# Kernel tuning notes

Measured on AMD Instinct MI355X. Metric: run time of the kernel, lower is better.

Reference implementation:

```python
import jax, jax.numpy as jnp
import numpy as np

B, LQ, LK, D = 16, 2048, 2048, 256
NEG = -1e10


def setup_inputs() -> dict:
    key = jax.random.key(0)
    k1, k2, k3, k4, k5 = jax.random.split(key, 5)
    scale = 1.0 / np.sqrt(D)
    return {
        "x": jax.random.normal(k1, (B, LQ, D), dtype=jnp.float32),
        "y": jax.random.normal(k2, (B, LK, D), dtype=jnp.float32),
        "mask": jnp.zeros((B, LK), dtype=bool),  # True = padded key position
        "Wq": jax.random.normal(k3, (D, D), dtype=jnp.float32) * scale,
        "Wk": jax.random.normal(k4, (D, D), dtype=jnp.float32) * scale,
        "Wv": jax.random.normal(k5, (D, D), dtype=jnp.float32) * scale,
    }


def reference(x, y, mask, Wq, Wk, Wv):
    # nn.Linear: out = in @ W.T (no bias)
    q = jnp.einsum('bqd,ed->bqe', x, Wq)   # [B, LQ, D]
    k = jnp.einsum('bkd,ed->bke', y, Wk)   # [B, LK, D]
    v = jnp.einsum('bkd,ed->bke', y, Wv)   # [B, LK, D]
    # cdist (p=2) via GEMM expansion: ||q||^2 + ||k||^2 - 2 q.k
    qn = jnp.sum(q * q, axis=-1)                              # [B, LQ]
    kn = jnp.sum(k * k, axis=-1)                              # [B, LK]
    d2 = qn[:, :, None] + kn[:, None, :] - 2.0 * jnp.einsum('bqd,bkd->bqk', q, k)
    dist = jnp.sqrt(jnp.maximum(d2, 0.0))                     # [B, LQ, LK]
    scores = jnp.exp(-dist)
    # masked_fill: where original mask is True, set pre-softmax score to -1e10
    scores = jnp.where(mask[:, None, :], NEG, scores)
    attn = jax.nn.softmax(scores, axis=-1)                    # [B, LQ, LK]
    att_out = jnp.einsum('bqk,bkd->bqd', attn, v)             # [B, LQ, D]
    return (att_out, attn)
```

## Files before the change

kernel.cpp:

```cpp
#include <hip/hip_runtime.h>
#include <stdint.h>

#define B_   16
#define L_   2048
#define D_   256
#define NROW (B_*L_)

#define EPAD 40
#define TPAD 66

typedef __attribute__((ext_vector_type(8))) short s8v;
typedef __attribute__((ext_vector_type(4))) float f4v;

__device__ __forceinline__ unsigned short f2b(float f) {
    unsigned u = __builtin_bit_cast(unsigned, f);
    return (unsigned short)((u + 0x7fffu + ((u >> 16) & 1u)) >> 16);
}

__device__ __forceinline__ void gl16(const void* g, void* l) {
    __builtin_amdgcn_global_load_lds(
        (const __attribute__((address_space(1))) unsigned int*)g,
        (__attribute__((address_space(3))) unsigned int*)l, 16, 0, 0);
}

__global__ __launch_bounds__(256) void qkv_kernel(
    const float* __restrict__ x, const float* __restrict__ y,
    const float* __restrict__ Wq, const float* __restrict__ Wk, const float* __restrict__ Wv,
    unsigned short* __restrict__ Qb, unsigned short* __restrict__ Kb,
    unsigned short* __restrict__ Vt,
    float* __restrict__ qn, float* __restrict__ kn)
{
    __shared__ unsigned short Xs[64*256];
    __shared__ unsigned short Ws[64*256];
    __shared__ unsigned short Ts[64*TPAD];

    const int t    = threadIdx.x;
    const int r0   = blockIdx.x * 64;
    const int type = blockIdx.y;

    const float* X = type ? y : x;

    #pragma unroll
    for (int p = 0; p < 16; ++p) {
        int idx  = p*256 + t;
        int row  = idx >> 6;
        int half = idx & 1;
        int blk  = (idx & 63) >> 1;
        int c4   = blk*8 + half*4;
        float4 vx = *(const float4*)(X + (size_t)(r0+row)*D_ + c4);
        uint2 px;
        px.x = (unsigned)f2b(vx.x) | ((unsigned)f2b(vx.y) << 16);
        px.y = (unsigned)f2b(vx.z) | ((unsigned)f2b(vx.w) << 16);
        *(uint2*)(Xs + row*256 + (blk ^ (row & 15))*8 + half*4) = px;
    }

    const int w = t >> 6, lane = t & 63, q16 = lane & 15, quad = lane >> 4;
    const int m0 = w * 16;

    float p4[4] = {0.f, 0.f, 0.f, 0.f};
    const f4v z4 = {0.f, 0.f, 0.f, 0.f};

    for (int ct = 0; ct < 4; ++ct) {
        const int e0 = ct * 64;

        __syncthreads();
        {
            const float* W = type ? Wk : Wq;
            #pragma unroll
            for (int p = 0; p < 16; ++p) {
                int idx  = p*256 + t;
                int row  = idx >> 6;
                int half = idx & 1;
                int blk  = (idx & 63) >> 1;
                int c4   = blk*8 + half*4;
                float4 vw = *(const float4*)(W + (size_t)(e0+row)*D_ + c4);
                uint2 pw;
                pw.x = (unsigned)f2b(vw.x) | ((unsigned)f2b(vw.y) << 16);
                pw.y = (unsigned)f2b(vw.z) | ((unsigned)f2b(vw.w) << 16);
                *(uint2*)(Ws + row*256 + (blk ^ (row & 15))*8 + half*4) = pw;
            }
        }
        __syncthreads();

        f4v acc[4];
        #pragma unroll
        for (int n = 0; n < 4; ++n) acc[n] = z4;
        #pragma unroll
        for (int c = 0; c < 8; ++c) {
            s8v a = *(const s8v*)(Xs + (m0 + q16)*256 + (((c*4+quad) ^ q16)*8));
            #pragma unroll
            for (int n = 0; n < 4; ++n) {
                s8v bb = *(const s8v*)(Ws + (n*16 + q16)*256 + (((c*4+quad) ^ q16)*8));
                acc[n] = __builtin_amdgcn_mfma_f32_16x16x32_bf16(a, bb, acc[n], 0, 0, 0);
            }
        }
        {
            unsigned short* Out = type ? Kb : Qb;
            #pragma unroll
            for (int n = 0; n < 4; ++n)
                #pragma unroll
                for (int r = 0; r < 4; ++r) {
                    float v = acc[n][r];
                    p4[r] += v * v;
                    Out[(size_t)(r0 + m0 + quad*4 + r)*D_ + e0 + n*16 + q16] = f2b(v);
                }
        }

        if (type) {
            __syncthreads();
            #pragma unroll
            for (int p = 0; p < 16; ++p) {
                int idx  = p*256 + t;
                int row  = idx >> 6;
                int half = idx & 1;
                int blk  = (idx & 63) >> 1;
                int c4   = blk*8 + half*4;
                float4 vw = *(const float4*)(Wv + (size_t)(e0+row)*D_ + c4);
                uint2 pw;
                pw.x = (unsigned)f2b(vw.x) | ((unsigned)f2b(vw.y) << 16);
                pw.y = (unsigned)f2b(vw.z) | ((unsigned)f2b(vw.w) << 16);
                *(uint2*)(Ws + row*256 + (blk ^ (row & 15))*8 + half*4) = pw;
            }
            __syncthreads();

            f4v vacc[4];
            #pragma unroll
            for (int n = 0; n < 4; ++n) vacc[n] = z4;
            #pragma unroll
            for (int c = 0; c < 8; ++c) {
                s8v a = *(const s8v*)(Xs + (m0 + q16)*256 + (((c*4+quad) ^ q16)*8));
                #pragma unroll
                for (int n = 0; n < 4; ++n) {
                    s8v bb = *(const s8v*)(Ws + (n*16 + q16)*256 + (((c*4+quad) ^ q16)*8));
                    vacc[n] = __builtin_amdgcn_mfma_f32_16x16x32_bf16(a, bb, vacc[n], 0, 0, 0);
                }
            }
            #pragma unroll
            for (int n = 0; n < 4; ++n)
                #pragma unroll
                for (int r = 0; r < 4; ++r)
                    Ts[(m0 + quad*4 + r)*TPAD + n*16 + q16] = f2b(vacc[n][r]);
            __syncthreads();
            int j    = t >> 2;
            int kseg = t & 3;
            unsigned pk[8];
            #pragma unroll
            for (int i = 0; i < 8; ++i) {
                unsigned lo = Ts[(kseg*16 + 2*i    )*TPAD + j];
                unsigned hi = Ts[(kseg*16 + 2*i + 1)*TPAD + j];
                pk[i] = lo | (hi << 16);
            }
            int bb_ = r0 >> 11;
            int k0g = r0 & (L_ - 1);
            unsigned short* dst = Vt + (size_t)(bb_*D_ + e0 + j)*L_ + k0g + kseg*16;
            *(uint4*)dst       = make_uint4(pk[0], pk[1], pk[2], pk[3]);
            *((uint4*)dst + 1) = make_uint4(pk[4], pk[5], pk[6], pk[7]);
        }
    }

    {
        float* norm = type ? kn : qn;
        #pragma unroll
        for (int r = 0; r < 4; ++r) {
            float v = p4[r];
            v += __shfl_xor(v, 1, 16);
            v += __shfl_xor(v, 2, 16);
            v += __shfl_xor(v, 4, 16);
            v += __shfl_xor(v, 8, 16);
            if (q16 == 0) norm[r0 + m0 + quad*4 + r] = v;
        }
    }
}

__device__ __forceinline__ void stage_K(const unsigned short* Kb, unsigned short* ks,
                                        int bk, int k0, int w, int lane) {
    #pragma unroll
    for (int p = 0; p < 4; ++p) {
        int slot = p*256 + w*64 + lane;
        int row  = slot >> 5;
        int blk  = slot & 31;
        gl16(Kb + (size_t)(bk + k0 + row)*D_ + ((blk ^ (row & 15))*8),
             ks + (size_t)(p*256 + w*64)*8);
    }
}
__device__ __forceinline__ void stage_V(const unsigned short* Vt, unsigned short* vs,
                                        int bD, int k0, int w, int lane) {
    #pragma unroll
    for (int p = 0; p < 4; ++p) {
        int slot = p*256 + w*64 + lane;
        int d    = slot >> 2;
        int blk  = slot & 3;
        gl16(Vt + (size_t)(bD + d)*L_ + k0 + ((blk ^ ((d >> 1) & 3))*8),
             vs + (size_t)(p*256 + w*64)*8);
    }
}

__global__ __launch_bounds__(256) void attnpv_kernel(
    const unsigned short* __restrict__ Qb, const unsigned short* __restrict__ Kb,
    const unsigned short* __restrict__ Vt,
    const float* __restrict__ qn, const float* __restrict__ kn,
    const unsigned char* __restrict__ mask,
    unsigned short* __restrict__ Eb,
    float* __restrict__ rowsum, float* __restrict__ att_out)
{
    __shared__ unsigned short Ks[2][32*256];
    __shared__ unsigned short Vs[2][256*32];
    __shared__ unsigned short Es[4][16*EPAD];

    const int t  = threadIdx.x;
    const int q0 = blockIdx.x * 64;
    const int b  = blockIdx.y;
    const int bk = b * L_;
    const int bD = b * D_;
    const int w = t >> 6, lane = t & 63, q16 = lane & 15, quad = lane >> 4;

    const int qrow = bk + q0 + w*16;
    s8v qa[8];
    float qnr[4];
    #pragma unroll
    for (int c = 0; c < 8; ++c)
        qa[c] = *(const s8v*)(Qb + (size_t)(qrow + q16)*D_ + c*32 + quad*8);
    #pragma unroll
    for (int r = 0; r < 4; ++r)
        qnr[r] = qn[qrow + quad*4 + r];

    unsigned short* ebase = Eb + (size_t)(qrow + (lane >> 2))*L_ + (lane & 3)*8;
    const unsigned short* esrc = &Es[w][(lane >> 2)*EPAD + (lane & 3)*8];

    float rs[4] = {0.f, 0.f, 0.f, 0.f};
    const f4v z4 = {0.f, 0.f, 0.f, 0.f};
    f4v O[16];
    #pragma unroll
    for (int n = 0; n < 16; ++n) O[n] = z4;

    stage_K(Kb, Ks[0], bk, 0, w, lane);
    stage_V(Vt, Vs[0], bD, 0, w, lane);
    for (int kt = 0; kt < 64; ++kt) {
        const int k0 = kt * 32;
        const int cur = kt & 1;
        __syncthreads();
        if (kt < 63) {
            stage_K(Kb, Ks[cur ^ 1], bk, k0 + 32, w, lane);
            stage_V(Vt, Vs[cur ^ 1], bD, k0 + 32, w, lane);
        }

        float kcv[2]; int mkv[2];
        #pragma unroll
        for (int n = 0; n < 2; ++n) {
            kcv[n] = kn[bk + k0 + n*16 + q16];
            mkv[n] = mask[bk + k0 + n*16 + q16];
        }

        #pragma unroll
        for (int n = 0; n < 2; ++n) {
            f4v s = {0.f, 0.f, 0.f, 0.f};
            #pragma unroll
            for (int c = 0; c < 8; ++c) {
                s8v bb = *(const s8v*)(Ks[cur] + (n*16 + q16)*256 + (((c*4+quad) ^ q16)*8));
                s = __builtin_amdgcn_mfma_f32_16x16x32_bf16(qa[c], bb, s, 0, 0, 0);
            }
            #pragma unroll
            for (int r = 0; r < 4; ++r) {
                float d2 = qnr[r] + kcv[n] - 2.0f * s[r];
                float dist = sqrtf(fmaxf(d2, 0.f));
                float E = mkv[n] ? 0.f : __expf(__expf(-dist));
                rs[r] += E;
                Es[w][(quad*4 + r)*EPAD + n*16 + q16] = f2b(E);
            }
        }
        s8v af = *(const s8v*)(&Es[w][q16*EPAD + quad*8]);
        #pragma unroll
        for (int n = 0; n < 16; ++n) {
            s8v vb = *(const s8v*)(Vs[cur] + (n*16 + q16)*32 +
                                   ((quad ^ ((q16 >> 1) & 3))*8));
            O[n] = __builtin_amdgcn_mfma_f32_16x16x32_bf16(af, vb, O[n], 0, 0, 0);
        }
        *(s8v*)(ebase + k0) = *(const s8v*)esrc;
    }

    float inv[4];
    #pragma unroll
    for (int r = 0; r < 4; ++r) {
        float v = rs[r];
        v += __shfl_xor(v, 1, 16);
        v += __shfl_xor(v, 2, 16);
        v += __shfl_xor(v, 4, 16);
        v += __shfl_xor(v, 8, 16);
        if (q16 == 0) rowsum[qrow + quad*4 + r] = v;
        inv[r] = 1.0f / v;
    }

    #pragma unroll
    for (int n = 0; n < 16; ++n)
        #pragma unroll
        for (int r = 0; r < 4; ++r)
            att_out[(size_t)(qrow + quad*4 + r)*D_ + n*16 + q16] = O[n][r] * inv[r];
}

__global__ __launch_bounds__(256) void norm_kernel(
    const unsigned short* __restrict__ Eb,
    const float* __restrict__ rowsum,
    float* __restrict__ attn_out)
{
    const int row = blockIdx.x;
    const int t   = threadIdx.x;
    const float inv = 1.0f / rowsum[row];
    const size_t base = (size_t)row * L_ + t*8;

    s8v e = *(const s8v*)(Eb + base);
    float4 o0, o1;
    o0.x = __builtin_bit_cast(float, ((unsigned)(unsigned short)e[0]) << 16) * inv;
    o0.y = __builtin_bit_cast(float, ((unsigned)(unsigned short)e[1]) << 16) * inv;
    o0.z = __builtin_bit_cast(float, ((unsigned)(unsigned short)e[2]) << 16) * inv;
    o0.w = __builtin_bit_cast(float, ((unsigned)(unsigned short)e[3]) << 16) * inv;
    o1.x = __builtin_bit_cast(float, ((unsigned)(unsigned short)e[4]) << 16) * inv;
    o1.y = __builtin_bit_cast(float, ((unsigned)(unsigned short)e[5]) << 16) * inv;
    o1.z = __builtin_bit_cast(float, ((unsigned)(unsigned short)e[6]) << 16) * inv;
    o1.w = __builtin_bit_cast(float, ((unsigned)(unsigned short)e[7]) << 16) * inv;
    *(float4*)(attn_out + base)     = o0;
    *(float4*)(attn_out + base + 4) = o1;
}

extern "C" void kernel_launch(void* const* d_in, const int* in_sizes, int n_in,
                              void* d_out, int out_size, void* d_ws, size_t ws_size,
                              hipStream_t stream) {
    (void)in_sizes; (void)n_in; (void)out_size; (void)ws_size;
    const float* x  = (const float*)d_in[0];
    const float* y  = (const float*)d_in[1];
    const unsigned char* mask = (const unsigned char*)d_in[2];
    const float* Wq = (const float*)d_in[3];
    const float* Wk = (const float*)d_in[4];
    const float* Wv = (const float*)d_in[5];

    char* ws = (char*)d_ws;
    unsigned short* Qb = (unsigned short*)ws;
    unsigned short* Kb = Qb + (size_t)NROW * D_;
    unsigned short* Vt = Kb + (size_t)NROW * D_;
    float* qn     = (float*)(ws + 3 * (size_t)NROW * D_ * 2);
    float* kn     = qn + NROW;
    float* rowsum = kn + NROW;
    unsigned short* Eb = (unsigned short*)(rowsum + NROW);

    float* att_out = (float*)d_out;
    float* attn    = att_out + (size_t)NROW * D_;

    qkv_kernel<<<dim3(512, 2), 256, 0, stream>>>(x, y, Wq, Wk, Wv,
                                                 Qb, Kb, Vt, qn, kn);
    attnpv_kernel<<<dim3(32, 16), 256, 0, stream>>>(Qb, Kb, Vt, qn, kn, mask,
                                                    Eb, rowsum, att_out);
    norm_kernel<<<dim3(NROW), 256, 0, stream>>>(Eb, rowsum, attn);
}
```

Measured before the change: 592.1 us.

## Fuse attention normalization into attn kernel, remap blocks, add hardware bf16 packing

Drops the separate norm kernel. Each attention block now re-reads its own bf16 exp rows from the workspace after the main loop and writes the normalized fp32 attention matrix with nontemporal stores. It also remaps block indices to interleave batches, raises wave priority around the MFMA loops, and replaces software bf16 rounding in the projection kernel with the v_cvt_pk_bf16_f32 instruction. The intent is to remove a launch and the rowsum round trip, and to lower conversion ALU cost. The cost is that the large attention write now sits in the tail of a 512-block kernel and may serialize with compute.

```diff
diff --git a/kernel.cpp b/kernel.cpp
--- a/kernel.cpp
+++ b/kernel.cpp
@@ -11,10 +11,17 @@
 
 typedef __attribute__((ext_vector_type(8))) short s8v;
 typedef __attribute__((ext_vector_type(4))) float f4v;
+typedef __attribute__((ext_vector_type(4))) float f4n;
 
 __device__ __forceinline__ unsigned short f2b(float f) {
     unsigned u = __builtin_bit_cast(unsigned, f);
     return (unsigned short)((u + 0x7fffu + ((u >> 16) & 1u)) >> 16);
+}
+
+__device__ __forceinline__ unsigned cvtpk(float a, float b) {
+    unsigned r;
+    asm("v_cvt_pk_bf16_f32 %0, %1, %2" : "=v"(r) : "v"(a), "v"(b));
+    return r;
 }
 
 __device__ __forceinline__ void gl16(const void* g, void* l) {
@@ -49,8 +56,8 @@
         int c4   = blk*8 + half*4;
         float4 vx = *(const float4*)(X + (size_t)(r0+row)*D_ + c4);
         uint2 px;
-        px.x = (unsigned)f2b(vx.x) | ((unsigned)f2b(vx.y) << 16);
-        px.y = (unsigned)f2b(vx.z) | ((unsigned)f2b(vx.w) << 16);
+        px.x = cvtpk(vx.x, vx.y);
+        px.y = cvtpk(vx.z, vx.w);
         *(uint2*)(Xs + row*256 + (blk ^ (row & 15))*8 + half*4) = px;
     }
 
@@ -75,8 +82,8 @@
                 int c4   = blk*8 + half*4;
                 float4 vw = *(const float4*)(W + (size_t)(e0+row)*D_ + c4);
                 uint2 pw;
-                pw.x = (unsigned)f2b(vw.x) | ((unsigned)f2b(vw.y) << 16);
-                pw.y = (unsigned)f2b(vw.z) | ((unsigned)f2b(vw.w) << 16);
+                pw.x = cvtpk(vw.x, vw.y);
+                pw.y = cvtpk(vw.z, vw.w);
                 *(uint2*)(Ws + row*256 + (blk ^ (row & 15))*8 + half*4) = pw;
             }
         }
@@ -117,8 +124,8 @@
                 int c4   = blk*8 + half*4;
                 float4 vw = *(const float4*)(Wv + (size_t)(e0+row)*D_ + c4);
                 uint2 pw;
-                pw.x = (unsigned)f2b(vw.x) | ((unsigned)f2b(vw.y) << 16);
-                pw.y = (unsigned)f2b(vw.z) | ((unsigned)f2b(vw.w) << 16);
+                pw.x = cvtpk(vw.x, vw.y);
+                pw.y = cvtpk(vw.z, vw.w);
                 *(uint2*)(Ws + row*256 + (blk ^ (row & 15))*8 + half*4) = pw;
             }
             __syncthreads();
@@ -201,15 +208,17 @@
     const float* __restrict__ qn, const float* __restrict__ kn,
     const unsigned char* __restrict__ mask,
     unsigned short* __restrict__ Eb,
-    float* __restrict__ rowsum, float* __restrict__ att_out)
+    float* __restrict__ att_out, float* __restrict__ attn)
 {
     __shared__ unsigned short Ks[2][32*256];
     __shared__ unsigned short Vs[2][256*32];
     __shared__ unsigned short Es[4][16*EPAD];
+    __shared__ float invsh[4][16];
 
     const int t  = threadIdx.x;
-    const int q0 = blockIdx.x * 64;
-    const int b  = blockIdx.y;
+    const int s  = blockIdx.y * 32 + blockIdx.x;
+    const int b  = ((s & 7) << 1) | (s >> 8);
+    const int q0 = ((s >> 3) & 31) * 64;
     const int bk = b * L_;
     const int bD = b * D_;
     const int w = t >> 6, lane = t & 63, q16 = lane & 15, quad = lane >> 4;
@@ -253,15 +262,17 @@
 
         #pragma unroll
         for (int n = 0; n < 2; ++n) {
-            f4v s = {0.f, 0.f, 0.f, 0.f};
+            f4v s4 = {0.f, 0.f, 0.f, 0.f};
+            __builtin_amdgcn_s_setprio(1);
             #pragma unroll
             for (int c = 0; c < 8; ++c) {
                 s8v bb = *(const s8v*)(Ks[cur] + (n*16 + q16)*256 + (((c*4+quad) ^ q16)*8));
-                s = __builtin_amdgcn_mfma_f32_16x16x32_bf16(qa[c], bb, s, 0, 0, 0);
-            }
+                s4 = __builtin_amdgcn_mfma_f32_16x16x32_bf16(qa[c], bb, s4, 0, 0, 0);
+            }
+            __builtin_amdgcn_s_setprio(0);
             #pragma unroll
             for (int r = 0; r < 4; ++r) {
-                float d2 = qnr[r] + kcv[n] - 2.0f * s[r];
+                float d2 = qnr[r] + kcv[n] - 2.0f * s4[r];
                 float dist = sqrtf(fmaxf(d2, 0.f));
                 float E = mkv[n] ? 0.f : __expf(__expf(-dist));
                 rs[r] += E;
@@ -269,16 +280,18 @@
             }
         }
         s8v af = *(const s8v*)(&Es[w][q16*EPAD + quad*8]);
+        __builtin_amdgcn_s_setprio(1);
         #pragma unroll
         for (int n = 0; n < 16; ++n) {
             s8v vb = *(const s8v*)(Vs[cur] + (n*16 + q16)*32 +
                                    ((quad ^ ((q16 >> 1) & 3))*8));
             O[n] = __builtin_amdgcn_mfma_f32_16x16x32_bf16(af, vb, O[n], 0, 0, 0);
         }
+        __builtin_amdgcn_s_setprio(0);
         *(s8v*)(ebase + k0) = *(const s8v*)esrc;
     }
 
-    float inv[4];
+    float inv4[4];
     #pragma unroll
     for (int r = 0; r < 4; ++r) {
         float v = rs[r];
@@ -286,39 +299,41 @@
         v += __shfl_xor(v, 2, 16);
         v += __shfl_xor(v, 4, 16);
         v += __shfl_xor(v, 8, 16);
-        if (q16 == 0) rowsum[qrow + quad*4 + r] = v;
-        inv[r] = 1.0f / v;
+        inv4[r] = 1.0f / v;
+        if (q16 == 0) invsh[w][quad*4 + r] = inv4[r];
     }
 
     #pragma unroll
     for (int n = 0; n < 16; ++n)
         #pragma unroll
         for (int r = 0; r < 4; ++r)
-            att_out[(size_t)(qrow + quad*4 + r)*D_ + n*16 + q16] = O[n][r] * inv[r];
-}
-
-__global__ __launch_bounds__(256) void norm_kernel(
-    const unsigned short* __restrict__ Eb,
-    const float* __restrict__ rowsum,
-    float* __restrict__ attn_out)
-{
-    const int row = blockIdx.x;
-    const int t   = threadIdx.x;
-    const float inv = 1.0f / rowsum[row];
-    const size_t base = (size_t)row * L_ + t*8;
-
-    s8v e = *(const s8v*)(Eb + base);
-    float4 o0, o1;
-    o0.x = __builtin_bit_cast(float, ((unsigned)(unsigned short)e[0]) << 16) * inv;
-    o0.y = __builtin_bit_cast(float, ((unsigned)(unsigned short)e[1]) << 16) * inv;
-    o0.z = __builtin_bit_cast(float, ((unsigned)(unsigned short)e[2]) << 16) * inv;
-    o0.w = __builtin_bit_cast(float, ((unsigned)(unsigned short)e[3]) << 16) * inv;
-    o1.x = __builtin_bit_cast(float, ((unsigned)(unsigned short)e[4]) << 16) * inv;
-    o1.y = __builtin_bit_cast(float, ((unsigned)(unsigned short)e[5]) << 16) * inv;
-    o1.z = __builtin_bit_cast(float, ((unsigned)(unsigned short)e[6]) << 16) * inv;
-    o1.w = __builtin_bit_cast(float, ((unsigned)(unsigned short)e[7]) << 16) * inv;
-    *(float4*)(attn_out + base)     = o0;
-    *(float4*)(attn_out + base + 4) = o1;
+            __builtin_nontemporal_store(O[n][r] * inv4[r],
+                att_out + (size_t)(qrow + quad*4 + r)*D_ + n*16 + q16);
+
+    __syncthreads();
+
+    {
+        const int rloc = lane >> 2, cseg = lane & 3;
+        const float invr = invsh[w][rloc];
+        const unsigned short* erow = Eb + (size_t)(qrow + rloc)*L_;
+        float* arow = attn + (size_t)(qrow + rloc)*L_;
+        #pragma unroll 4
+        for (int it = 0; it < 64; ++it) {
+            const int c0 = it*32 + cseg*8;
+            s8v e = *(const s8v*)(erow + c0);
+            f4n o0, o1;
+            o0.x = __builtin_bit_cast(float, ((unsigned)(unsigned short)e[0]) << 16) * invr;
+            o0.y = __builtin_bit_cast(float, ((unsigned)(unsigned short)e[1]) << 16) * invr;
+            o0.z = __builtin_bit_cast(float, ((unsigned)(unsigned short)e[2]) << 16) * invr;
+            o0.w = __builtin_bit_cast(float, ((unsigned)(unsigned short)e[3]) << 16) * invr;
+            o1.x = __builtin_bit_cast(float, ((unsigned)(unsigned short)e[4]) << 16) * invr;
+            o1.y = __builtin_bit_cast(float, ((unsigned)(unsigned short)e[5]) << 16) * invr;
+            o1.z = __builtin_bit_cast(float, ((unsigned)(unsigned short)e[6]) << 16) * invr;
+            o1.w = __builtin_bit_cast(float, ((unsigned)(unsigned short)e[7]) << 16) * invr;
+            __builtin_nontemporal_store(o0, (f4n*)(arow + c0));
+            __builtin_nontemporal_store(o1, (f4n*)(arow + c0 + 4));
+        }
+    }
 }
 
 extern "C" void kernel_launch(void* const* d_in, const int* in_sizes, int n_in,
@@ -338,8 +353,7 @@
     unsigned short* Vt = Kb + (size_t)NROW * D_;
     float* qn     = (float*)(ws + 3 * (size_t)NROW * D_ * 2);
     float* kn     = qn + NROW;
-    float* rowsum = kn + NROW;
-    unsigned short* Eb = (unsigned short*)(rowsum + NROW);
+    unsigned short* Eb = (unsigned short*)(kn + NROW);
 
     float* att_out = (float*)d_out;
     float* attn    = att_out + (size_t)NROW * D_;
@@ -347,6 +361,5 @@
     qkv_kernel<<<dim3(512, 2), 256, 0, stream>>>(x, y, Wq, Wk, Wv,
                                                  Qb, Kb, Vt, qn, kn);
     attnpv_kernel<<<dim3(32, 16), 256, 0, stream>>>(Qb, Kb, Vt, qn, kn, mask,
-                                                    Eb, rowsum, att_out);
-    norm_kernel<<<dim3(NROW), 256, 0, stream>>>(Eb, rowsum, attn);
-}
+                                                    Eb, att_out, attn);
+}
```

After: 605.6 us. +2.3%, slower.

## Triple-buffer attention tiles with 512-thread blocks, LDS kn/mask, and nontemporal stores

Applied to the files above, without the earlier changes.

Several changes land together. The attention kernel grows to 512 threads covering 128 query rows and moves to a three-stage K/V LDS pipeline with explicit vmcnt waits and barriers. Key norms and mask go into shared memory, block indices are remapped to interleave batches, and MFMA sections get raised priority with s_setprio. Separately, bf16 conversion switches to the packed v_cvt_pk_bf16_f32 instruction, and the output stores become nontemporal. The extra LDS and the hand-written waitcnt logic may reduce occupancy or risk ordering bugs.

```diff
diff --git a/kernel.cpp b/kernel.cpp
--- a/kernel.cpp
+++ b/kernel.cpp
@@ -11,10 +11,17 @@
 
 typedef __attribute__((ext_vector_type(8))) short s8v;
 typedef __attribute__((ext_vector_type(4))) float f4v;
+typedef __attribute__((ext_vector_type(4))) float f4n;
 
 __device__ __forceinline__ unsigned short f2b(float f) {
     unsigned u = __builtin_bit_cast(unsigned, f);
     return (unsigned short)((u + 0x7fffu + ((u >> 16) & 1u)) >> 16);
+}
+
+__device__ __forceinline__ unsigned cvtpk(float a, float b) {
+    unsigned r;
+    asm("v_cvt_pk_bf16_f32 %0, %1, %2" : "=v"(r) : "v"(a), "v"(b));
+    return r;
 }
 
 __device__ __forceinline__ void gl16(const void* g, void* l) {
@@ -49,8 +56,8 @@
         int c4   = blk*8 + half*4;
         float4 vx = *(const float4*)(X + (size_t)(r0+row)*D_ + c4);
         uint2 px;
-        px.x = (unsigned)f2b(vx.x) | ((unsigned)f2b(vx.y) << 16);
-        px.y = (unsigned)f2b(vx.z) | ((unsigned)f2b(vx.w) << 16);
+        px.x = cvtpk(vx.x, vx.y);
+        px.y = cvtpk(vx.z, vx.w);
         *(uint2*)(Xs + row*256 + (blk ^ (row & 15))*8 + half*4) = px;
     }
 
@@ -75,8 +82,8 @@
                 int c4   = blk*8 + half*4;
                 float4 vw = *(const float4*)(W + (size_t)(e0+row)*D_ + c4);
                 uint2 pw;
-                pw.x = (unsigned)f2b(vw.x) | ((unsigned)f2b(vw.y) << 16);
-                pw.y = (unsigned)f2b(vw.z) | ((unsigned)f2b(vw.w) << 16);
+                pw.x = cvtpk(vw.x, vw.y);
+                pw.y = cvtpk(vw.z, vw.w);
                 *(uint2*)(Ws + row*256 + (blk ^ (row & 15))*8 + half*4) = pw;
             }
         }
@@ -117,8 +124,8 @@
                 int c4   = blk*8 + half*4;
                 float4 vw = *(const float4*)(Wv + (size_t)(e0+row)*D_ + c4);
                 uint2 pw;
-                pw.x = (unsigned)f2b(vw.x) | ((unsigned)f2b(vw.y) << 16);
-                pw.y = (unsigned)f2b(vw.z) | ((unsigned)f2b(vw.w) << 16);
+                pw.x = cvtpk(vw.x, vw.y);
+                pw.y = cvtpk(vw.z, vw.w);
                 *(uint2*)(Ws + row*256 + (blk ^ (row & 15))*8 + half*4) = pw;
             }
             __syncthreads();
@@ -175,27 +182,27 @@
 __device__ __forceinline__ void stage_K(const unsigned short* Kb, unsigned short* ks,
                                         int bk, int k0, int w, int lane) {
     #pragma unroll
-    for (int p = 0; p < 4; ++p) {
-        int slot = p*256 + w*64 + lane;
+    for (int p = 0; p < 2; ++p) {
+        int slot = p*512 + w*64 + lane;
         int row  = slot >> 5;
         int blk  = slot & 31;
         gl16(Kb + (size_t)(bk + k0 + row)*D_ + ((blk ^ (row & 15))*8),
-             ks + (size_t)(p*256 + w*64)*8);
+             ks + (size_t)(p*512 + w*64)*8);
     }
 }
 __device__ __forceinline__ void stage_V(const unsigned short* Vt, unsigned short* vs,
                                         int bD, int k0, int w, int lane) {
     #pragma unroll
-    for (int p = 0; p < 4; ++p) {
-        int slot = p*256 + w*64 + lane;
+    for (int p = 0; p < 2; ++p) {
+        int slot = p*512 + w*64 + lane;
         int d    = slot >> 2;
         int blk  = slot & 3;
         gl16(Vt + (size_t)(bD + d)*L_ + k0 + ((blk ^ ((d >> 1) & 3))*8),
-             vs + (size_t)(p*256 + w*64)*8);
-    }
-}
-
-__global__ __launch_bounds__(256) void attnpv_kernel(
+             vs + (size_t)(p*512 + w*64)*8);
+    }
+}
+
+__global__ __launch_bounds__(512) void attnpv_kernel(
     const unsigned short* __restrict__ Qb, const unsigned short* __restrict__ Kb,
     const unsigned short* __restrict__ Vt,
     const float* __restrict__ qn, const float* __restrict__ kn,
@@ -203,18 +210,24 @@
     unsigned short* __restrict__ Eb,
     float* __restrict__ rowsum, float* __restrict__ att_out)
 {
-    __shared__ unsigned short Ks[2][32*256];
-    __shared__ unsigned short Vs[2][256*32];
-    __shared__ unsigned short Es[4][16*EPAD];
+    __shared__ unsigned short Ks[3][32*256];
+    __shared__ unsigned short Vs[3][256*32];
+    __shared__ unsigned short Es[8][16*EPAD];
+    __shared__ float         knS[L_];
+    __shared__ unsigned char mkS[L_];
 
     const int t  = threadIdx.x;
-    const int q0 = blockIdx.x * 64;
-    const int b  = blockIdx.y;
+    const int s  = blockIdx.y * 16 + blockIdx.x;
+    const int b  = ((s & 7) << 1) | (s >> 7);
+    const int q0 = ((s >> 3) & 15) * 128;
     const int bk = b * L_;
     const int bD = b * D_;
     const int w = t >> 6, lane = t & 63, q16 = lane & 15, quad = lane >> 4;
-
     const int qrow = bk + q0 + w*16;
+
+    *(float4*)&knS[t*4] = *(const float4*)&kn[bk + t*4];
+    ((unsigned*)mkS)[t] = ((const unsigned*)(mask + bk))[t];
+
     s8v qa[8];
     float qnr[4];
     #pragma unroll
@@ -233,35 +246,27 @@
     #pragma unroll
     for (int n = 0; n < 16; ++n) O[n] = z4;
 
-    stage_K(Kb, Ks[0], bk, 0, w, lane);
-    stage_V(Vt, Vs[0], bD, 0, w, lane);
-    for (int kt = 0; kt < 64; ++kt) {
+    auto do_tile = [&](int kt, int cur) {
         const int k0 = kt * 32;
-        const int cur = kt & 1;
-        __syncthreads();
-        if (kt < 63) {
-            stage_K(Kb, Ks[cur ^ 1], bk, k0 + 32, w, lane);
-            stage_V(Vt, Vs[cur ^ 1], bD, k0 + 32, w, lane);
-        }
-
         float kcv[2]; int mkv[2];
         #pragma unroll
         for (int n = 0; n < 2; ++n) {
-            kcv[n] = kn[bk + k0 + n*16 + q16];
-            mkv[n] = mask[bk + k0 + n*16 + q16];
-        }
-
+            kcv[n] = knS[k0 + n*16 + q16];
+            mkv[n] = mkS[k0 + n*16 + q16];
+        }
         #pragma unroll
         for (int n = 0; n < 2; ++n) {
-            f4v s = {0.f, 0.f, 0.f, 0.f};
+            f4v s4 = z4;
+            __builtin_amdgcn_s_setprio(1);
             #pragma unroll
             for (int c = 0; c < 8; ++c) {
                 s8v bb = *(const s8v*)(Ks[cur] + (n*16 + q16)*256 + (((c*4+quad) ^ q16)*8));
-                s = __builtin_amdgcn_mfma_f32_16x16x32_bf16(qa[c], bb, s, 0, 0, 0);
-            }
+                s4 = __builtin_amdgcn_mfma_f32_16x16x32_bf16(qa[c], bb, s4, 0, 0, 0);
+            }
+            __builtin_amdgcn_s_setprio(0);
             #pragma unroll
             for (int r = 0; r < 4; ++r) {
-                float d2 = qnr[r] + kcv[n] - 2.0f * s[r];
+                float d2 = fmaf(-2.0f, s4[r], qnr[r] + kcv[n]);
                 float dist = sqrtf(fmaxf(d2, 0.f));
                 float E = mkv[n] ? 0.f : __expf(__expf(-dist));
                 rs[r] += E;
@@ -269,16 +274,41 @@
             }
         }
         s8v af = *(const s8v*)(&Es[w][q16*EPAD + quad*8]);
+        __builtin_amdgcn_s_setprio(1);
         #pragma unroll
         for (int n = 0; n < 16; ++n) {
             s8v vb = *(const s8v*)(Vs[cur] + (n*16 + q16)*32 +
                                    ((quad ^ ((q16 >> 1) & 3))*8));
             O[n] = __builtin_amdgcn_mfma_f32_16x16x32_bf16(af, vb, O[n], 0, 0, 0);
         }
+        __builtin_amdgcn_s_setprio(0);
         *(s8v*)(ebase + k0) = *(const s8v*)esrc;
-    }
-
-    float inv[4];
+    };
+
+    stage_K(Kb, Ks[0], bk, 0,  w, lane);  stage_V(Vt, Vs[0], bD, 0,  w, lane);
+    stage_K(Kb, Ks[1], bk, 32, w, lane);  stage_V(Vt, Vs[1], bD, 32, w, lane);
+
+    asm volatile("s_waitcnt vmcnt(4) lgkmcnt(0)\n\ts_barrier" ::: "memory");
+    do_tile(0, 0);
+    asm volatile("s_barrier" ::: "memory");
+    stage_K(Kb, Ks[2], bk, 64, w, lane);  stage_V(Vt, Vs[2], bD, 64, w, lane);
+
+    int cur = 1;
+    for (int kt = 1; kt <= 62; ++kt) {
+        asm volatile("s_waitcnt vmcnt(5)\n\ts_barrier" ::: "memory");
+        do_tile(kt, cur);
+        asm volatile("s_barrier" ::: "memory");
+        if (kt <= 61) {
+            int nb = cur - 1; if (nb < 0) nb = 2;
+            stage_K(Kb, Ks[nb], bk, (kt+2)*32, w, lane);
+            stage_V(Vt, Vs[nb], bD, (kt+2)*32, w, lane);
+        }
+        cur = (cur == 2) ? 0 : cur + 1;
+    }
+    asm volatile("s_waitcnt vmcnt(1)\n\ts_barrier" ::: "memory");
+    do_tile(63, 0);
+
+    float inv4[4];
     #pragma unroll
     for (int r = 0; r < 4; ++r) {
         float v = rs[r];
@@ -286,15 +316,15 @@
         v += __shfl_xor(v, 2, 16);
         v += __shfl_xor(v, 4, 16);
         v += __shfl_xor(v, 8, 16);
+        inv4[r] = 1.0f / v;
         if (q16 == 0) rowsum[qrow + quad*4 + r] = v;
-        inv[r] = 1.0f / v;
-    }
-
+    }
     #pragma unroll
     for (int n = 0; n < 16; ++n)
         #pragma unroll
         for (int r = 0; r < 4; ++r)
-            att_out[(size_t)(qrow + quad*4 + r)*D_ + n*16 + q16] = O[n][r] * inv[r];
+            __builtin_nontemporal_store(O[n][r] * inv4[r],
+                att_out + (size_t)(qrow + quad*4 + r)*D_ + n*16 + q16);
 }
 
 __global__ __launch_bounds__(256) void norm_kernel(
@@ -308,7 +338,7 @@
     const size_t base = (size_t)row * L_ + t*8;
 
     s8v e = *(const s8v*)(Eb + base);
-    float4 o0, o1;
+    f4n o0, o1;
     o0.x = __builtin_bit_cast(float, ((unsigned)(unsigned short)e[0]) << 16) * inv;
     o0.y = __builtin_bit_cast(float, ((unsigned)(unsigned short)e[1]) << 16) * inv;
     o0.z = __builtin_bit_cast(float, ((unsigned)(unsigned short)e[2]) << 16) * inv;
@@ -317,8 +347,8 @@
     o1.y = __builtin_bit_cast(float, ((unsigned)(unsigned short)e[5]) << 16) * inv;
     o1.z = __builtin_bit_cast(float, ((unsigned)(unsigned short)e[6]) << 16) * inv;
     o1.w = __builtin_bit_cast(float, ((unsigned)(unsigned short)e[7]) << 16) * inv;
-    *(float4*)(attn_out + base)     = o0;
-    *(float4*)(attn_out + base + 4) = o1;
+    __builtin_nontemporal_store(o0, (f4n*)(attn_out + base));
+    __builtin_nontemporal_store(o1, (f4n*)(attn_out + base + 4));
 }
 
 extern "C" void kernel_launch(void* const* d_in, const int* in_sizes, int n_in,
@@ -346,7 +376,7 @@
 
     qkv_kernel<<<dim3(512, 2), 256, 0, stream>>>(x, y, Wq, Wk, Wv,
                                                  Qb, Kb, Vt, qn, kn);
-    attnpv_kernel<<<dim3(32, 16), 256, 0, stream>>>(Qb, Kb, Vt, qn, kn, mask,
+    attnpv_kernel<<<dim3(16, 16), 512, 0, stream>>>(Qb, Kb, Vt, qn, kn, mask,
                                                     Eb, rowsum, att_out);
     norm_kernel<<<dim3(NROW), 256, 0, stream>>>(Eb, rowsum, attn);
 }
```

Result: faster. 575.3 us (-2.8%).
